# Kernel optimization log

Measured on AMD Instinct MI355X. Metric: run time of the kernel, lower is better.

Reference implementation:

```python
import jax, jax.numpy as jnp
import numpy as np

EPS = 1e-6

def elu_feature_map(x):
    return jax.nn.elu(x) + 1.0

def setup_inputs() -> dict:
    key = jax.random.key(0)
    kq, kk, kv = jax.random.split(key, 3)
    B, N, L, S, H, D, M = 4, 8, 1024, 1024, 8, 64, 64
    queries = jax.random.normal(kq, (B, N, L, H, D), dtype=jnp.float32)
    keys = jax.random.normal(kk, (B, N, S, H, D), dtype=jnp.float32)
    values = jax.random.normal(kv, (B, N, S, H, M), dtype=jnp.float32)
    key_mask = jnp.ones((B, S), dtype=jnp.float32)  # key_lengths.float_matrix (all valid)
    return {"queries": queries, "keys": keys, "values": values, "key_mask": key_mask}

def reference(queries, keys, values, key_mask):
    # Q: [B,N,L,H,D], K: [B,N,S,H,D], V: [B,N,S,H,M], key_mask: [B,S]
    Q = elu_feature_map(queries)
    K = elu_feature_map(keys) * key_mask[:, None, :, None, None]
    # KV state: [B,N,H,M,D]
    KV = jnp.einsum('bnshd,bnshm->bnhmd', K, values)
    # normalizer: [B,N,L,H]
    Z = 1.0 / (jnp.einsum('bnlhd,bnhd->bnlh', Q, K.sum(axis=2)) + EPS)
    # output: [B,N,L,H,M]
    V = jnp.einsum('bnlhd,bnhmd,bnlh->bnlhm', Q, KV, Z)
    return V
```

## Files before the change

### kernel.cpp

```cpp
#include <hip/hip_runtime.h>
#include <hip/hip_bf16.h>


constexpr int Bc = 4, Nc = 8, Hc = 8;
constexpr int Lc = 1024, Sc = 1024, Dc = 64, Mc = 64;
constexpr int HD = Hc * Dc;
constexpr int GROUPS = Bc * Nc * Hc;
constexpr int LSPLITS = 4;
constexpr int LROWS = Lc / LSPLITS;
constexpr int PARTIAL = Dc * Mc + Dc;
constexpr int NTL = LROWS / 64;
constexpr int PADD = 68;
constexpr float EPSF = 1e-6f;

typedef __attribute__((ext_vector_type(8))) __bf16 bf16x8;
typedef __attribute__((ext_vector_type(4))) float f32x4;

__device__ __forceinline__ float elup1(float x) {
    return x > 0.0f ? x + 1.0f : __expf(x);
}
__device__ __forceinline__ unsigned short f2bf(float f) {
    unsigned u = __builtin_bit_cast(unsigned, f);
    u += 0x7fffu + ((u >> 16) & 1u);
    return (unsigned short)(u >> 16);
}
__device__ __forceinline__ float bf2f(unsigned short h) {
    return __builtin_bit_cast(float, (unsigned)h << 16);
}
__device__ __forceinline__ void splitbf(float x, unsigned short& h, unsigned short& l) {
    h = f2bf(x);
    l = f2bf(x - bf2f(h));
}
__device__ __forceinline__ unsigned pack2(unsigned short lo, unsigned short hi) {
    return (unsigned)lo | ((unsigned)hi << 16);
}
__device__ __forceinline__ bf16x8 ones_frag() {
    union { bf16x8 v; unsigned short s[8]; } u;
    #pragma unroll
    for (int i = 0; i < 8; ++i) u.s[i] = 0x3F80;
    return u.v;
}

template<int NSPL>
__global__ void __launch_bounds__(256, 4)
la_kv_direct(const float* __restrict__ Kg, const float* __restrict__ Vg,
             const float* __restrict__ Mg, float* __restrict__ ws)
{
    constexpr int SR = Sc / NSPL;
    constexpr int NT = SR / 32;

    const int t    = threadIdx.x;
    const int lane = t & 63;
    const int w    = t >> 6;
    const int frow = lane & 15;
    const int kg   = lane >> 4;
    const int g    = blockIdx.y;
    const int sp   = blockIdx.x;
    const int h    = g & 7;
    const int bn   = g >> 3;
    const int b    = g >> 6;

    const size_t rowbase = (size_t)bn * Sc * HD + (size_t)h * Dc;
    const size_t mbase   = (size_t)b * Sc;
    const int    sbase   = sp * SR;

    f32x4 acc[4], aks;
    #pragma unroll
    for (int ms = 0; ms < 4; ++ms) acc[ms] = (f32x4){0.f, 0.f, 0.f, 0.f};
    aks = (f32x4){0.f, 0.f, 0.f, 0.f};
    const bf16x8 ones = ones_frag();

    union uf { bf16x8 v; unsigned short s[8]; };

    #pragma unroll 1
    for (int it = 0; it < NT; ++it) {
        const int sb = sbase + it * 32 + 8 * kg;
        const float* kp = Kg + rowbase + (size_t)sb * HD + 16 * w + frow;
        const float* vp = Vg + rowbase + (size_t)sb * HD + frow;
        const float* mp = Mg + mbase + sb;

        float ka[8], mk[8], vb[4][8];
        #pragma unroll
        for (int j = 0; j < 8; ++j) {
            ka[j] = kp[j * HD];
            mk[j] = mp[j];
        }
        #pragma unroll
        for (int ms = 0; ms < 4; ++ms)
            #pragma unroll
            for (int j = 0; j < 8; ++j)
                vb[ms][j] = vp[j * HD + 16 * ms];

        uf kh, kl;
        #pragma unroll
        for (int j = 0; j < 8; ++j) {
            const float a = elup1(ka[j]) * mk[j];
            splitbf(a, kh.s[j], kl.s[j]);
        }
        aks = __builtin_amdgcn_mfma_f32_16x16x32_bf16(kh.v, ones, aks, 0, 0, 0);
        aks = __builtin_amdgcn_mfma_f32_16x16x32_bf16(kl.v, ones, aks, 0, 0, 0);
        #pragma unroll
        for (int ms = 0; ms < 4; ++ms) {
            uf vh, vl;
            #pragma unroll
            for (int j = 0; j < 8; ++j)
                splitbf(vb[ms][j], vh.s[j], vl.s[j]);
            acc[ms] = __builtin_amdgcn_mfma_f32_16x16x32_bf16(kh.v, vh.v, acc[ms], 0, 0, 0);
            acc[ms] = __builtin_amdgcn_mfma_f32_16x16x32_bf16(kh.v, vl.v, acc[ms], 0, 0, 0);
            acc[ms] = __builtin_amdgcn_mfma_f32_16x16x32_bf16(kl.v, vh.v, acc[ms], 0, 0, 0);
        }
    }

    float* outp = ws + (size_t)(g * NSPL + sp) * PARTIAL;
    #pragma unroll
    for (int ms = 0; ms < 4; ++ms)
        #pragma unroll
        for (int r = 0; r < 4; ++r)
            outp[(16 * w + 4 * (lane >> 4) + r) * Mc + 16 * ms + frow] = acc[ms][r];

    if (frow == 0) {
        #pragma unroll
        for (int r = 0; r < 4; ++r)
            outp[Dc * Mc + 16 * w + 4 * (lane >> 4) + r] = aks[r];
    }
}

template<int NSPL>
__global__ void __launch_bounds__(256, 4)
la_out_mfma(const float* __restrict__ Qg, const float* __restrict__ ws,
            float* __restrict__ Og)
{
    __shared__ unsigned short kvh[Mc][PADD];
    __shared__ unsigned short kvl[Mc][PADD];
    __shared__ unsigned short ksh[64];
    __shared__ unsigned short ksl[64];
    __shared__ unsigned short qhh[64][PADD];
    __shared__ unsigned short qll[64][PADD];

    const int t    = threadIdx.x;
    const int tx   = t & 15;
    const int tyq  = t >> 4;
    const int lane = t & 63;
    const int w    = t >> 6;
    const int g    = blockIdx.y;
    const int ls   = blockIdx.x;
    const int h    = g & 7;
    const int bn   = g >> 3;

    const size_t rowbase = (size_t)bn * Lc * HD + (size_t)h * Dc;
    const float* pw = ws + (size_t)g * NSPL * PARTIAL;
    const int lbase = ls * LROWS;

    float4 qr[4];
    auto loadB = [&](int it) {
        const int l0 = lbase + it * 64 + 4 * tyq;
        #pragma unroll
        for (int j = 0; j < 4; ++j)
            qr[j] = *reinterpret_cast<const float4*>(Qg + rowbase + (size_t)(l0 + j) * HD + 4 * tx);
    };
    auto storeB = [&]() {
        #pragma unroll
        for (int j = 0; j < 4; ++j) {
            const int r = 4 * tyq + j;
            const float q[4] = {qr[j].x, qr[j].y, qr[j].z, qr[j].w};
            unsigned short h0, l0, h1, l1, h2, l2, h3, l3;
            splitbf(elup1(q[0]), h0, l0);
            splitbf(elup1(q[1]), h1, l1);
            splitbf(elup1(q[2]), h2, l2);
            splitbf(elup1(q[3]), h3, l3);
            uint2 ph, pl;
            ph.x = pack2(h0, h1); ph.y = pack2(h2, h3);
            pl.x = pack2(l0, l1); pl.y = pack2(l2, l3);
            *reinterpret_cast<uint2*>(&qhh[r][4 * tx]) = ph;
            *reinterpret_cast<uint2*>(&qll[r][4 * tx]) = pl;
        }
    };

    loadB(0);
    #pragma unroll
    for (int e = 0; e < 16; ++e) {
        const int idx = t + 256 * e;
        float s = 0.f;
        #pragma unroll
        for (int sp = 0; sp < NSPL; ++sp) s += pw[sp * PARTIAL + idx];
        unsigned short hh, ll;
        splitbf(s, hh, ll);
        kvh[idx & 63][idx >> 6] = hh;
        kvl[idx & 63][idx >> 6] = ll;
    }
    if (t < 64) {
        float s = 0.f;
        #pragma unroll
        for (int sp = 0; sp < NSPL; ++sp) s += pw[sp * PARTIAL + Dc * Mc + t];
        unsigned short hh, ll;
        splitbf(s, hh, ll);
        ksh[t] = hh;
        ksl[t] = ll;
    }
    storeB();
    __syncthreads();

    const int fcol = 8 * (lane >> 4);
    const int frow = lane & 15;
    const size_t obase = (size_t)bn * Lc * HD + (size_t)h * Mc;

    for (int it = 0; it < NTL; ++it) {
        if (it + 1 < NTL) loadB(it + 1);
        union { bf16x8 v; uint2 u[2]; } fah0, fal0, fah1, fal1;
        {
            const uint2* p;
            p = reinterpret_cast<const uint2*>(&qhh[16 * w + frow][fcol]);      fah0.u[0] = p[0]; fah0.u[1] = p[1];
            p = reinterpret_cast<const uint2*>(&qll[16 * w + frow][fcol]);      fal0.u[0] = p[0]; fal0.u[1] = p[1];
            p = reinterpret_cast<const uint2*>(&qhh[16 * w + frow][32 + fcol]); fah1.u[0] = p[0]; fah1.u[1] = p[1];
            p = reinterpret_cast<const uint2*>(&qll[16 * w + frow][32 + fcol]); fal1.u[0] = p[0]; fal1.u[1] = p[1];
        }
        f32x4 acc[4], accz;
        #pragma unroll
        for (int ms = 0; ms < 4; ++ms) acc[ms] = (f32x4){0.f, 0.f, 0.f, 0.f};
        accz = (f32x4){0.f, 0.f, 0.f, 0.f};

        #pragma unroll
        for (int ks = 0; ks < 2; ++ks) {
            const bf16x8 fh = ks ? fah1.v : fah0.v;
            const bf16x8 fl = ks ? fal1.v : fal0.v;
            #pragma unroll
            for (int ms = 0; ms < 4; ++ms) {
                union { bf16x8 v; uint2 u[2]; } fbh, fbl;
                const uint2* ph = reinterpret_cast<const uint2*>(&kvh[16 * ms + frow][32 * ks + fcol]);
                fbh.u[0] = ph[0]; fbh.u[1] = ph[1];
                const uint2* pl = reinterpret_cast<const uint2*>(&kvl[16 * ms + frow][32 * ks + fcol]);
                fbl.u[0] = pl[0]; fbl.u[1] = pl[1];
                acc[ms] = __builtin_amdgcn_mfma_f32_16x16x32_bf16(fh, fbh.v, acc[ms], 0, 0, 0);
                acc[ms] = __builtin_amdgcn_mfma_f32_16x16x32_bf16(fh, fbl.v, acc[ms], 0, 0, 0);
                acc[ms] = __builtin_amdgcn_mfma_f32_16x16x32_bf16(fl, fbh.v, acc[ms], 0, 0, 0);
            }
            union { bf16x8 v; uint2 u[2]; } fzh, fzl;
            const uint2* ph = reinterpret_cast<const uint2*>(&ksh[32 * ks + fcol]);
            fzh.u[0] = ph[0]; fzh.u[1] = ph[1];
            const uint2* pl = reinterpret_cast<const uint2*>(&ksl[32 * ks + fcol]);
            fzl.u[0] = pl[0]; fzl.u[1] = pl[1];
            accz = __builtin_amdgcn_mfma_f32_16x16x32_bf16(fh, fzh.v, accz, 0, 0, 0);
            accz = __builtin_amdgcn_mfma_f32_16x16x32_bf16(fh, fzl.v, accz, 0, 0, 0);
            accz = __builtin_amdgcn_mfma_f32_16x16x32_bf16(fl, fzh.v, accz, 0, 0, 0);
        }

        const int lt = lbase + it * 64 + 16 * w + 4 * (lane >> 4);
        #pragma unroll
        for (int r = 0; r < 4; ++r) {
            const float z = 1.0f / (accz[r] + EPSF);
            const size_t ro = obase + (size_t)(lt + r) * HD + frow;
            #pragma unroll
            for (int ms = 0; ms < 4; ++ms)
                Og[ro + 16 * ms] = acc[ms][r] * z;
        }
        __syncthreads();
        if (it + 1 < NTL) storeB();
        __syncthreads();
    }
}

__global__ void __launch_bounds__(256, 1)
la_fused_kernel(const float* __restrict__ Qg, const float* __restrict__ Kg,
                const float* __restrict__ Vg, const float* __restrict__ Mg,
                float* __restrict__ Og)
{
    __shared__ float lk[32][Dc];
    __shared__ float lv[32][Mc];
    __shared__ float kvt[Dc][Mc];
    __shared__ float ksm[Dc];
    __shared__ float qt[Dc][64];

    const int t  = threadIdx.x;
    const int tx = t & 15;
    const int ty = t >> 4;
    const int g  = blockIdx.x;
    const int h  = g & 7;
    const int bn = g >> 3;
    const int b  = g >> 6;

    const size_t rowbase = (size_t)bn * Sc * HD + (size_t)h * Dc;
    const size_t mbase   = (size_t)b * Sc;

    const int d0 = tx * 4, m0 = ty * 4, c4 = tx * 4, r0 = ty;

    float acc[4][4] = {{0.f,0.f,0.f,0.f},{0.f,0.f,0.f,0.f},{0.f,0.f,0.f,0.f},{0.f,0.f,0.f,0.f}};
    float ks[4] = {0.f, 0.f, 0.f, 0.f};
    float4 kr[2], vr[2];
    float  mr[2];

    auto loadA = [&](int it) {
        const int s0 = it * 32;
        #pragma unroll
        for (int k = 0; k < 2; ++k) {
            const int r = r0 + 16 * k;
            const size_t off = rowbase + (size_t)(s0 + r) * HD + c4;
            kr[k] = *reinterpret_cast<const float4*>(Kg + off);
            vr[k] = *reinterpret_cast<const float4*>(Vg + off);
            mr[k] = Mg[mbase + s0 + r];
        }
    };
    auto storeA = [&]() {
        #pragma unroll
        for (int k = 0; k < 2; ++k) {
            const int r = r0 + 16 * k;
            float4 kk;
            kk.x = elup1(kr[k].x) * mr[k];
            kk.y = elup1(kr[k].y) * mr[k];
            kk.z = elup1(kr[k].z) * mr[k];
            kk.w = elup1(kr[k].w) * mr[k];
            *reinterpret_cast<float4*>(&lk[r][c4]) = kk;
            *reinterpret_cast<float4*>(&lv[r][c4]) = vr[k];
        }
    };

    loadA(0);
    storeA();
    __syncthreads();
    for (int it = 0; it < Sc / 32; ++it) {
        if (it + 1 < Sc / 32) loadA(it + 1);
        #pragma unroll 8
        for (int r = 0; r < 32; ++r) {
            const float4 k4 = *reinterpret_cast<const float4*>(&lk[r][d0]);
            const float4 v4 = *reinterpret_cast<const float4*>(&lv[r][m0]);
            const float kk[4] = {k4.x, k4.y, k4.z, k4.w};
            const float vv[4] = {v4.x, v4.y, v4.z, v4.w};
            ks[0] += kk[0]; ks[1] += kk[1]; ks[2] += kk[2]; ks[3] += kk[3];
            #pragma unroll
            for (int i = 0; i < 4; ++i)
                #pragma unroll
                for (int j = 0; j < 4; ++j)
                    acc[i][j] += kk[i] * vv[j];
        }
        __syncthreads();
        if (it + 1 < Sc / 32) storeA();
        __syncthreads();
    }

    #pragma unroll
    for (int i = 0; i < 4; ++i) {
        float4 w;
        w.x = acc[i][0]; w.y = acc[i][1]; w.z = acc[i][2]; w.w = acc[i][3];
        *reinterpret_cast<float4*>(&kvt[d0 + i][m0]) = w;
    }
    if (ty == 0) {
        #pragma unroll
        for (int i = 0; i < 4; ++i) ksm[d0 + i] = ks[i];
    }
    __syncthreads();

    float4 qr[4];
    auto loadB = [&](int it) {
        const int l0 = it * 64;
        #pragma unroll
        for (int k = 0; k < 4; ++k) {
            const int r = r0 + 16 * k;
            const size_t off = rowbase + (size_t)(l0 + r) * HD + c4;
            qr[k] = *reinterpret_cast<const float4*>(Qg + off);
        }
    };
    const int swzw = (tx & 7) << 2;
    auto storeB = [&]() {
        #pragma unroll
        for (int k = 0; k < 4; ++k) {
            const int r = r0 + 16 * k;
            const int lidx = r ^ swzw;
            qt[c4 + 0][lidx] = elup1(qr[k].x);
            qt[c4 + 1][lidx] = elup1(qr[k].y);
            qt[c4 + 2][lidx] = elup1(qr[k].z);
            qt[c4 + 3][lidx] = elup1(qr[k].w);
        }
    };

    loadB(0);
    storeB();
    __syncthreads();
    for (int it = 0; it < Lc / 64; ++it) {
        if (it + 1 < Lc / 64) loadB(it + 1);
        float accB[4][4] = {{0.f,0.f,0.f,0.f},{0.f,0.f,0.f,0.f},{0.f,0.f,0.f,0.f},{0.f,0.f,0.f,0.f}};
        float za[4] = {0.f, 0.f, 0.f, 0.f};
        #pragma unroll 8
        for (int d = 0; d < Dc; ++d) {
            const int swz = ((d >> 2) & 7) << 2;
            const float4 q4  = *reinterpret_cast<const float4*>(&qt[d][(4 * ty) ^ swz]);
            const float4 kv4 = *reinterpret_cast<const float4*>(&kvt[d][4 * tx]);
            const float kd = ksm[d];
            const float qq[4] = {q4.x, q4.y, q4.z, q4.w};
            const float kv[4] = {kv4.x, kv4.y, kv4.z, kv4.w};
            #pragma unroll
            for (int i = 0; i < 4; ++i) {
                za[i] += qq[i] * kd;
                #pragma unroll
                for (int j = 0; j < 4; ++j)
                    accB[i][j] += qq[i] * kv[j];
            }
        }
        const int l0 = it * 64;
        const size_t obase = (size_t)bn * Lc * HD + (size_t)h * Mc;
        #pragma unroll
        for (int i = 0; i < 4; ++i) {
            const int l = l0 + 4 * ty + i;
            const float z = 1.0f / (za[i] + EPSF);
            float4 o;
            o.x = accB[i][0] * z; o.y = accB[i][1] * z;
            o.z = accB[i][2] * z; o.w = accB[i][3] * z;
            *reinterpret_cast<float4*>(Og + obase + (size_t)l * HD + 4 * tx) = o;
        }
        __syncthreads();
        if (it + 1 < Lc / 64) storeB();
        __syncthreads();
    }
}

extern "C" void kernel_launch(void* const* d_in, const int* in_sizes, int n_in,
                              void* d_out, int out_size, void* d_ws, size_t ws_size,
                              hipStream_t stream) {
    const float* Qg = (const float*)d_in[0];
    const float* Kg = (const float*)d_in[1];
    const float* Vg = (const float*)d_in[2];
    const float* Mg = (const float*)d_in[3];
    float* Og = (float*)d_out;

    const size_t need4 = (size_t)GROUPS * 4 * PARTIAL * sizeof(float);
    if (ws_size >= need4) {
        float* ws = (float*)d_ws;
        hipLaunchKernelGGL((la_kv_direct<4>), dim3(4, GROUPS), dim3(256), 0, stream,
                           Kg, Vg, Mg, ws);
        hipLaunchKernelGGL((la_out_mfma<4>), dim3(LSPLITS, GROUPS), dim3(256), 0, stream,
                           Qg, ws, Og);
    } else {
        hipLaunchKernelGGL(la_fused_kernel, dim3(GROUPS), dim3(256), 0, stream,
                           Qg, Kg, Vg, Mg, Og);
    }
}
```

Before: 80.89 us.

## Stage full K/V rows through LDS in KV kernel and add split reduction kernel

```diff
diff --git a/kernel.cpp b/kernel.cpp
--- a/kernel.cpp
+++ b/kernel.cpp
@@ -6,6 +6,7 @@
 constexpr int Lc = 1024, Sc = 1024, Dc = 64, Mc = 64;
 constexpr int HD = Hc * Dc;
 constexpr int GROUPS = Bc * Nc * Hc;
+constexpr int BN = Bc * Nc;
 constexpr int LSPLITS = 4;
 constexpr int LROWS = Lc / LSPLITS;
 constexpr int PARTIAL = Dc * Mc + Dc;
@@ -42,93 +43,151 @@
 }
 
 template<int NSPL>
-__global__ void __launch_bounds__(256, 4)
-la_kv_direct(const float* __restrict__ Kg, const float* __restrict__ Vg,
-             const float* __restrict__ Mg, float* __restrict__ ws)
+__global__ void __launch_bounds__(1024, 1)
+la_kv_fullrow2(const float* __restrict__ Kg, const float* __restrict__ Vg,
+               const float* __restrict__ Mg, float* __restrict__ ws)
 {
     constexpr int SR = Sc / NSPL;
     constexpr int NT = SR / 32;
 
-    const int t    = threadIdx.x;
-    const int lane = t & 63;
-    const int w    = t >> 6;
-    const int frow = lane & 15;
-    const int kg   = lane >> 4;
-    const int g    = blockIdx.y;
-    const int sp   = blockIdx.x;
-    const int h    = g & 7;
-    const int bn   = g >> 3;
-    const int b    = g >> 6;
-
-    const size_t rowbase = (size_t)bn * Sc * HD + (size_t)h * Dc;
-    const size_t mbase   = (size_t)b * Sc;
-    const int    sbase   = sp * SR;
-
-    f32x4 acc[4], aks;
+    __shared__ float tl[32][512];
+
+    const int t     = threadIdx.x;
+    const int lane  = t & 63;
+    const int w     = t >> 6;
+    const int h     = w >> 1;
+    const int dhalf = w & 1;
+    const int frow  = lane & 15;
+    const int kg    = lane >> 4;
+    const int bn    = blockIdx.y;
+    const int sp    = blockIdx.x;
+    const int b     = bn >> 3;
+
+    const size_t slab  = (size_t)bn * Sc * HD;
+    const size_t mbase = (size_t)b * Sc;
+    const int    sbase = sp * SR;
+
+    const int srow = t >> 7;
+    const int scol = (t & 127) * 4;
+
+    f32x4 acc[2][4];
+    f32x4 aks[2];
     #pragma unroll
-    for (int ms = 0; ms < 4; ++ms) acc[ms] = (f32x4){0.f, 0.f, 0.f, 0.f};
-    aks = (f32x4){0.f, 0.f, 0.f, 0.f};
+    for (int c = 0; c < 2; ++c) {
+        aks[c] = (f32x4){0.f, 0.f, 0.f, 0.f};
+        #pragma unroll
+        for (int ms = 0; ms < 4; ++ms) acc[c][ms] = (f32x4){0.f, 0.f, 0.f, 0.f};
+    }
     const bf16x8 ones = ones_frag();
-
     union uf { bf16x8 v; unsigned short s[8]; };
 
-    #pragma unroll 1
+    float4 stK[4], stV[4];
+    auto ldK = [&](int it) {
+        #pragma unroll
+        for (int q = 0; q < 4; ++q)
+            stK[q] = *reinterpret_cast<const float4*>(
+                Kg + slab + (size_t)(sbase + it * 32 + srow + 8 * q) * HD + scol);
+    };
+    auto ldV = [&](int it) {
+        #pragma unroll
+        for (int q = 0; q < 4; ++q)
+            stV[q] = *reinterpret_cast<const float4*>(
+                Vg + slab + (size_t)(sbase + it * 32 + srow + 8 * q) * HD + scol);
+    };
+
+    ldK(0);
     for (int it = 0; it < NT; ++it) {
-        const int sb = sbase + it * 32 + 8 * kg;
-        const float* kp = Kg + rowbase + (size_t)sb * HD + 16 * w + frow;
-        const float* vp = Vg + rowbase + (size_t)sb * HD + frow;
-        const float* mp = Mg + mbase + sb;
-
-        float ka[8], mk[8], vb[4][8];
-        #pragma unroll
-        for (int j = 0; j < 8; ++j) {
-            ka[j] = kp[j * HD];
-            mk[j] = mp[j];
-        }
-        #pragma unroll
-        for (int ms = 0; ms < 4; ++ms)
-            #pragma unroll
-            for (int j = 0; j < 8; ++j)
-                vb[ms][j] = vp[j * HD + 16 * ms];
-
-        uf kh, kl;
-        #pragma unroll
-        for (int j = 0; j < 8; ++j) {
-            const float a = elup1(ka[j]) * mk[j];
-            splitbf(a, kh.s[j], kl.s[j]);
-        }
-        aks = __builtin_amdgcn_mfma_f32_16x16x32_bf16(kh.v, ones, aks, 0, 0, 0);
-        aks = __builtin_amdgcn_mfma_f32_16x16x32_bf16(kl.v, ones, aks, 0, 0, 0);
+        #pragma unroll
+        for (int q = 0; q < 4; ++q)
+            *reinterpret_cast<float4*>(&tl[srow + 8 * q][scol]) = stK[q];
+        __syncthreads();
+        ldV(it);
+
+        const int s0 = sbase + it * 32;
+        float ml[8];
+        #pragma unroll
+        for (int j = 0; j < 8; ++j) ml[j] = Mg[mbase + s0 + 8 * kg + j];
+        uf kh[2], kl[2];
+        #pragma unroll
+        for (int c = 0; c < 2; ++c) {
+            #pragma unroll
+            for (int j = 0; j < 8; ++j) {
+                const float ka = tl[8 * kg + j][64 * h + 32 * dhalf + 16 * c + frow];
+                splitbf(elup1(ka) * ml[j], kh[c].s[j], kl[c].s[j]);
+            }
+            aks[c] = __builtin_amdgcn_mfma_f32_16x16x32_bf16(kh[c].v, ones, aks[c], 0, 0, 0);
+            aks[c] = __builtin_amdgcn_mfma_f32_16x16x32_bf16(kl[c].v, ones, aks[c], 0, 0, 0);
+        }
+        __syncthreads();
+
+        #pragma unroll
+        for (int q = 0; q < 4; ++q)
+            *reinterpret_cast<float4*>(&tl[srow + 8 * q][scol]) = stV[q];
+        __syncthreads();
+        if (it + 1 < NT) ldK(it + 1);
+
         #pragma unroll
         for (int ms = 0; ms < 4; ++ms) {
             uf vh, vl;
             #pragma unroll
-            for (int j = 0; j < 8; ++j)
-                splitbf(vb[ms][j], vh.s[j], vl.s[j]);
-            acc[ms] = __builtin_amdgcn_mfma_f32_16x16x32_bf16(kh.v, vh.v, acc[ms], 0, 0, 0);
-            acc[ms] = __builtin_amdgcn_mfma_f32_16x16x32_bf16(kh.v, vl.v, acc[ms], 0, 0, 0);
-            acc[ms] = __builtin_amdgcn_mfma_f32_16x16x32_bf16(kl.v, vh.v, acc[ms], 0, 0, 0);
-        }
-    }
-
-    float* outp = ws + (size_t)(g * NSPL + sp) * PARTIAL;
+            for (int j = 0; j < 8; ++j) {
+                const float vb = tl[8 * kg + j][64 * h + 16 * ms + frow];
+                splitbf(vb, vh.s[j], vl.s[j]);
+            }
+            #pragma unroll
+            for (int c = 0; c < 2; ++c) {
+                acc[c][ms] = __builtin_amdgcn_mfma_f32_16x16x32_bf16(kh[c].v, vh.v, acc[c][ms], 0, 0, 0);
+                acc[c][ms] = __builtin_amdgcn_mfma_f32_16x16x32_bf16(kh[c].v, vl.v, acc[c][ms], 0, 0, 0);
+                acc[c][ms] = __builtin_amdgcn_mfma_f32_16x16x32_bf16(kl[c].v, vh.v, acc[c][ms], 0, 0, 0);
+            }
+        }
+        __syncthreads();
+    }
+
+    float* outp = ws + (size_t)((bn * 8 + h) * NSPL + sp) * PARTIAL;
     #pragma unroll
-    for (int ms = 0; ms < 4; ++ms)
-        #pragma unroll
-        for (int r = 0; r < 4; ++r)
-            outp[(16 * w + 4 * (lane >> 4) + r) * Mc + 16 * ms + frow] = acc[ms][r];
+    for (int c = 0; c < 2; ++c)
+        #pragma unroll
+        for (int ms = 0; ms < 4; ++ms)
+            #pragma unroll
+            for (int r = 0; r < 4; ++r)
+                outp[(32 * dhalf + 16 * c + 4 * kg + r) * Mc + 16 * ms + frow] = acc[c][ms][r];
 
     if (frow == 0) {
         #pragma unroll
-        for (int r = 0; r < 4; ++r)
-            outp[Dc * Mc + 16 * w + 4 * (lane >> 4) + r] = aks[r];
+        for (int c = 0; c < 2; ++c)
+            #pragma unroll
+            for (int r = 0; r < 4; ++r)
+                outp[Dc * Mc + 32 * dhalf + 16 * c + 4 * kg + r] = aks[c][r];
     }
 }
 
 template<int NSPL>
+__global__ void __launch_bounds__(256, 8)
+la_reduce(float* __restrict__ ws)
+{
+    constexpr int NF4 = PARTIAL / 4;
+    constexpr int QW  = NF4 / 4;
+    const int g = blockIdx.y;
+    const int q = blockIdx.x;
+    const int t = threadIdx.x;
+
+    float4* base = reinterpret_cast<float4*>(ws + (size_t)g * NSPL * PARTIAL);
+    for (int i = q * QW + t; i < (q + 1) * QW; i += 256) {
+        float4 s = base[i];
+        #pragma unroll
+        for (int sp = 1; sp < NSPL; ++sp) {
+            const float4 p = base[sp * NF4 + i];
+            s.x += p.x; s.y += p.y; s.z += p.z; s.w += p.w;
+        }
+        base[i] = s;
+    }
+}
+
+template<int NSUM>
 __global__ void __launch_bounds__(256, 4)
 la_out_mfma(const float* __restrict__ Qg, const float* __restrict__ ws,
-            float* __restrict__ Og)
+            float* __restrict__ Og, int pstride)
 {
     __shared__ unsigned short kvh[Mc][PADD];
     __shared__ unsigned short kvl[Mc][PADD];
@@ -148,7 +207,7 @@
     const int bn   = g >> 3;
 
     const size_t rowbase = (size_t)bn * Lc * HD + (size_t)h * Dc;
-    const float* pw = ws + (size_t)g * NSPL * PARTIAL;
+    const float* pw = ws + (size_t)g * pstride * PARTIAL;
     const int lbase = ls * LROWS;
 
     float4 qr[4];
@@ -182,7 +241,7 @@
         const int idx = t + 256 * e;
         float s = 0.f;
         #pragma unroll
-        for (int sp = 0; sp < NSPL; ++sp) s += pw[sp * PARTIAL + idx];
+        for (int sp = 0; sp < NSUM; ++sp) s += pw[sp * PARTIAL + idx];
         unsigned short hh, ll;
         splitbf(s, hh, ll);
         kvh[idx & 63][idx >> 6] = hh;
@@ -191,7 +250,7 @@
     if (t < 64) {
         float s = 0.f;
         #pragma unroll
-        for (int sp = 0; sp < NSPL; ++sp) s += pw[sp * PARTIAL + Dc * Mc + t];
+        for (int sp = 0; sp < NSUM; ++sp) s += pw[sp * PARTIAL + Dc * Mc + t];
         unsigned short hh, ll;
         splitbf(s, hh, ll);
         ksh[t] = hh;
@@ -420,13 +479,15 @@
     const float* Mg = (const float*)d_in[3];
     float* Og = (float*)d_out;
 
-    const size_t need4 = (size_t)GROUPS * 4 * PARTIAL * sizeof(float);
-    if (ws_size >= need4) {
+    const size_t need8 = (size_t)GROUPS * 8 * PARTIAL * sizeof(float);
+    if (ws_size >= need8) {
         float* ws = (float*)d_ws;
-        hipLaunchKernelGGL((la_kv_direct<4>), dim3(4, GROUPS), dim3(256), 0, stream,
+        hipLaunchKernelGGL((la_kv_fullrow2<8>), dim3(8, BN), dim3(1024), 0, stream,
                            Kg, Vg, Mg, ws);
-        hipLaunchKernelGGL((la_out_mfma<4>), dim3(LSPLITS, GROUPS), dim3(256), 0, stream,
-                           Qg, ws, Og);
+        hipLaunchKernelGGL((la_reduce<8>), dim3(4, GROUPS), dim3(256), 0, stream,
+                           ws);
+        hipLaunchKernelGGL((la_out_mfma<1>), dim3(LSPLITS, GROUPS), dim3(256), 0, stream,
+                           Qg, ws, Og, 8);
     } else {
         hipLaunchKernelGGL(la_fused_kernel, dim3(GROUPS), dim3(256), 0, stream,
                            Qg, Kg, Vg, Mg, Og);
```

Result: slower. 125.0 us (+54.6%).
